# Optimization experiments

Measured on AMD Instinct MI355X. Metric: run time of the kernel, lower is better.

The kernel has to match this reference:

```python
import jax, jax.numpy as jnp
import numpy as np

EPS = 1e-5
NEG_INF = -1e30

def layer_norm(x, g, b):
    mu = jnp.mean(x, axis=-1, keepdims=True)
    var = jnp.var(x, axis=-1, keepdims=True)
    return (x - mu) * jax.lax.rsqrt(var + EPS) * g + b

def setup_inputs() -> dict:
    B, L, D, H, F = 2, 2048, 1024, 16, 4096
    key = jax.random.key(0)
    ks = jax.random.split(key, 12)
    s = 0.02
    return {
        "x": jax.random.normal(ks[0], (B, L, D), jnp.float32),
        "torus_dist": jax.random.uniform(ks[1], (1, L, L), jnp.float32),
        "time_emb": jax.random.normal(ks[2], (B, D), jnp.float32),
        "mask": jnp.ones((B, L), dtype=bool),
        "ln1_g": jnp.ones((D,), jnp.float32),
        "ln1_b": jnp.zeros((D,), jnp.float32),
        "Wqkv": jax.random.normal(ks[3], (D, 3 * D), jnp.float32) * s,
        "Wout": jax.random.normal(ks[4], (D, D), jnp.float32) * s,
        "torus_scale": jnp.full((H,), 0.1, jnp.float32),
        "ln2_g": jnp.ones((D,), jnp.float32),
        "ln2_b": jnp.zeros((D,), jnp.float32),
        "W1": jax.random.normal(ks[5], (D, F), jnp.float32) * s,
        "b1": jnp.zeros((F,), jnp.float32),
        "W2": jax.random.normal(ks[6], (F, D), jnp.float32) * s,
        "b2": jnp.zeros((D,), jnp.float32),
        "Wt": jax.random.normal(ks[7], (D, 2 * D), jnp.float32) * s,
        "bt": jnp.zeros((2 * D,), jnp.float32),
    }

def reference(x, torus_dist, time_emb, mask, ln1_g, ln1_b, Wqkv, Wout,
              torus_scale, ln2_g, ln2_b, W1, b1, W2, b2, Wt, bt):
    B, L, D = x.shape
    H = torus_scale.shape[0]
    hd = D // H
    # AdaLN time modulation
    tp = jax.nn.gelu(time_emb) @ Wt + bt          # [B, 2D]
    scale, shift = jnp.split(tp, 2, axis=-1)
    h = layer_norm(x, ln1_g, ln1_b) * (1.0 + scale[:, None, :]) + shift[:, None, :]
    # QKV: [B, L, 3, H, hd]
    qkv = (h @ Wqkv).reshape(B, L, 3, H, hd)
    q = jnp.transpose(qkv[:, :, 0], (0, 2, 1, 3))  # [B, H, L, hd]
    k = jnp.transpose(qkv[:, :, 1], (0, 2, 1, 3))
    v = jnp.transpose(qkv[:, :, 2], (0, 2, 1, 3))
    scores = jnp.einsum('bhqd,bhkd->bhqk', q, k) / np.sqrt(hd).astype(np.float32)
    scores = scores - torus_dist[:, None, :, :] * torus_scale[None, :, None, None]
    pad = ~mask[:, None, None, :]                  # [B,1,1,L]
    scores = jnp.where(pad, NEG_INF, scores)
    attn = jax.nn.softmax(scores, axis=-1)
    attn = jnp.nan_to_num(attn, nan=0.0)
    out = jnp.einsum('bhqk,bhkd->bhqd', attn, v)
    out = jnp.transpose(out, (0, 2, 1, 3)).reshape(B, L, D)
    x = x + out @ Wout
    h2 = layer_norm(x, ln2_g, ln2_b)
    x = x + (jax.nn.gelu(h2 @ W1 + b1) @ W2 + b2)
    return x
```

## Files before the change

kernel.cpp:

```cpp
#include <hip/hip_runtime.h>

typedef unsigned short us16;
typedef __bf16 bf16x8 __attribute__((ext_vector_type(8)));
typedef float f32x2 __attribute__((ext_vector_type(2)));
typedef float f32x4 __attribute__((ext_vector_type(4)));
typedef float f32x16 __attribute__((ext_vector_type(16)));
typedef unsigned u32x4 __attribute__((ext_vector_type(4)));

#define DEV __device__ __forceinline__

DEV us16 f2bf(float x) {
  union { float f; unsigned u; } un; un.f = x;
  unsigned r = un.u + 0x7fffu + ((un.u >> 16) & 1u);
  return (us16)(r >> 16);
}
DEV float bf2f(us16 u) {
  union { unsigned u; float f; } x; x.u = ((unsigned)u) << 16; return x.f;
}
DEV float gelu_f(float x) {
  float u = 0.7978845608028654f * (x + 0.044715f * x * x * x);
  float e = __expf(2.0f * u);
  return x * (1.0f - 1.0f / (e + 1.0f));
}

DEV f32x16 mfma32(bf16x8 a, bf16x8 b, f32x16 c) {
  return __builtin_amdgcn_mfma_f32_32x32x16_bf16(a, b, c, 0, 0, 0);
}

DEV unsigned cvtpk_bf16(float lo, float hi) {
  unsigned r;
  asm("v_cvt_pk_bf16_f32 %0, %1, %2" : "=v"(r) : "v"(lo), "v"(hi));
  return r;
}
DEV void plswap(unsigned& x, unsigned& y) {
  asm("v_permlane32_swap_b32 %0, %1" : "+v"(x), "+v"(y));
}

DEV void gll16(const void* gp, void* lp) {
  __builtin_amdgcn_global_load_lds(
      (__attribute__((address_space(1))) unsigned int*)(unsigned long long)(gp),
      (__attribute__((address_space(3))) unsigned int*)(unsigned int)(unsigned long long)(lp),
      16, 0, 0);
}

__global__ __launch_bounds__(256) void prep_tp(const float* __restrict__ te,
                                               const float* __restrict__ Wt,
                                               const float* __restrict__ bt,
                                               float* __restrict__ tp) {
  __shared__ float ge[1024];
  __shared__ float red[256];
  const int b = blockIdx.y, jt = blockIdx.x, t = threadIdx.x;
  for (int i = t; i < 1024; i += 256) ge[i] = gelu_f(te[b * 1024 + i]);
  __syncthreads();
  const int j = jt * 64 + (t & 63);
  const int dg = t >> 6;
  float acc = 0.f;
  for (int i = 0; i < 256; ++i) {
    int d = dg * 256 + i;
    acc += ge[d] * Wt[(size_t)d * 2048 + j];
  }
  red[t] = acc;
  __syncthreads();
  if (t < 64) tp[b * 2048 + jt * 64 + t] =
      red[t] + red[64 + t] + red[128 + t] + red[192 + t] + bt[jt * 64 + t];
}

__global__ __launch_bounds__(256) void transpose_cast(const float* __restrict__ W,
                                                      us16* __restrict__ Wo,
                                                      int K, int N) {
  __shared__ float t[32][33];
  const int bn = blockIdx.x * 32, bk = blockIdx.y * 32;
  const int tx = threadIdx.x & 31, ty = threadIdx.x >> 5;
#pragma unroll
  for (int j = 0; j < 32; j += 8) t[ty + j][tx] = W[(size_t)(bk + ty + j) * N + bn + tx];
  __syncthreads();
#pragma unroll
  for (int j = 0; j < 32; j += 8) Wo[(size_t)(bn + ty + j) * K + bk + tx] = f2bf(t[tx][ty + j]);
}

template <int MOD>
__global__ __launch_bounds__(256) void ln_kernel(const float* __restrict__ x,
                                                 const float* __restrict__ gw,
                                                 const float* __restrict__ bw,
                                                 const float* __restrict__ tp,
                                                 us16* __restrict__ out) {
  const int row = blockIdx.x, b = row >> 11, t = threadIdx.x;
  const int lane = t & 63, wid = t >> 6;
  float4 xv = ((const float4*)(x + (size_t)row * 1024))[t];
  float s = xv.x + xv.y + xv.z + xv.w;
  float s2 = xv.x * xv.x + xv.y * xv.y + xv.z * xv.z + xv.w * xv.w;
#pragma unroll
  for (int o = 32; o; o >>= 1) { s += __shfl_xor(s, o); s2 += __shfl_xor(s2, o); }
  __shared__ float rs_[4], rq_[4];
  if (lane == 0) { rs_[wid] = s; rq_[wid] = s2; }
  __syncthreads();
  s = rs_[0] + rs_[1] + rs_[2] + rs_[3];
  s2 = rq_[0] + rq_[1] + rq_[2] + rq_[3];
  const float mu = s * 0.0009765625f;
  const float var = s2 * 0.0009765625f - mu * mu;
  const float rsig = rsqrtf(var + 1e-5f);
  float4 gv = ((const float4*)gw)[t], bv = ((const float4*)bw)[t];
  float y[4] = {(xv.x - mu) * rsig * gv.x + bv.x, (xv.y - mu) * rsig * gv.y + bv.y,
                (xv.z - mu) * rsig * gv.z + bv.z, (xv.w - mu) * rsig * gv.w + bv.w};
  if (MOD) {
    float4 sc = ((const float4*)(tp + b * 2048))[t];
    float4 sh = ((const float4*)(tp + b * 2048 + 1024))[t];
    y[0] = y[0] * (1.f + sc.x) + sh.x;
    y[1] = y[1] * (1.f + sc.y) + sh.y;
    y[2] = y[2] * (1.f + sc.z) + sh.z;
    y[3] = y[3] * (1.f + sc.w) + sh.w;
  }
  ushort4 o = {f2bf(y[0]), f2bf(y[1]), f2bf(y[2]), f2bf(y[3])};
  ((ushort4*)(out + (size_t)row * 1024))[t] = o;
}

__global__ __launch_bounds__(256) void permute_dist(const float* __restrict__ dist,
                                                    us16* __restrict__ dp) {
  const int Q = blockIdx.x >> 3, part = blockIdx.x & 7;
  for (int j = threadIdx.x; j < 2048; j += 256) {
    int i = part * 2048 + j;
    int l = i & 63, ks = (i >> 6) & 7, t = i >> 9;
    int row = Q * 32 + (l & 31);
    int col = t * 64 + ks * 8 + (l >> 5) * 4;
    float4 v = *(const float4*)(dist + (size_t)row * 2048 + col);
    ushort4 o = {f2bf(v.x), f2bf(v.y), f2bf(v.z), f2bf(v.w)};
    *(ushort4*)(dp + ((size_t)Q * 16384 + i) * 4) = o;
  }
}

__global__ __launch_bounds__(256) void transpose_v(const us16* __restrict__ v,
                                                   us16* __restrict__ vt) {
  __shared__ us16 t[64][72];
  const int bh = blockIdx.y, kv0 = blockIdx.x * 64;
  const int tid = threadIdx.x;
  const int r = tid >> 2, c0 = (tid & 3) * 16;
  const us16* src = v + ((size_t)bh * 2048 + kv0 + r) * 64 + c0;
  *(uint4*)&t[r][c0] = *(const uint4*)src;
  *(uint4*)&t[r][c0 + 8] = *(const uint4*)(src + 8);
  __syncthreads();
  const int d = tid >> 2, kvl = (tid & 3) * 16;
  us16 buf[16];
#pragma unroll
  for (int i = 0; i < 16; ++i) buf[i] = t[kvl + i][d];
  us16* dst = vt + ((size_t)bh * 64 + d) * 2048 + kv0 + kvl;
  *(uint4*)dst = *(uint4*)buf;
  *(uint4*)(dst + 8) = *(uint4*)(buf + 8);
}

template <int EPI>
__global__ __launch_bounds__(256) void gemm_bt(const us16* __restrict__ A,
                                               const us16* __restrict__ Bt,
                                               int M, int N, int K,
                                               const float* __restrict__ addf,
                                               const float* __restrict__ bias,
                                               float* __restrict__ outf,
                                               us16* __restrict__ outh,
                                               us16* __restrict__ qb,
                                               us16* __restrict__ kb,
                                               us16* __restrict__ vb) {
  __shared__ us16 Al[128 * 64];
  __shared__ us16 Bl[128 * 64];
  const int tid = threadIdx.x, lane = tid & 63, wid = tid >> 6;
  const int wm = wid >> 1, wn = wid & 1;
  const int nbx = gridDim.x, nwg = nbx * gridDim.y;
  const int idlin = blockIdx.y * nbx + blockIdx.x;
  const int wg = (idlin & 7) * (nwg >> 3) + (idlin >> 3);
  const int bm = wg / nbx, bn = wg % nbx;
  const int q31 = lane & 31, hi = lane >> 5;
  const int srow = lane >> 3;
  const int scol = ((lane & 7) ^ srow) << 3;

  f32x16 acc[2][2] = {};
  const size_t arow0 = (size_t)bm * 128 + wid * 32 + srow;
  const size_t brow0 = (size_t)bn * 128 + wid * 32 + srow;

  for (int k0 = 0; k0 < K; k0 += 64) {
#pragma unroll
    for (int j = 0; j < 4; ++j) {
      gll16(A + (arow0 + j * 8) * K + k0 + scol, (char*)Al + (wid * 32 + j * 8) * 128);
      gll16(Bt + (brow0 + j * 8) * K + k0 + scol, (char*)Bl + (wid * 32 + j * 8) * 128);
    }
    __syncthreads();
#pragma unroll
    for (int ks = 0; ks < 4; ++ks) {
      const int cb = ks * 32 + hi * 16;
      bf16x8 af[2], bfr[2];
#pragma unroll
      for (int i = 0; i < 2; ++i) {
        int ra = wm * 64 + i * 32 + q31;
        af[i] = *(const bf16x8*)((const char*)Al + ra * 128 + (cb ^ ((ra & 7) << 4)));
        int rb = wn * 64 + i * 32 + q31;
        bfr[i] = *(const bf16x8*)((const char*)Bl + rb * 128 + (cb ^ ((rb & 7) << 4)));
      }
#pragma unroll
      for (int mi = 0; mi < 2; ++mi)
#pragma unroll
        for (int ni = 0; ni < 2; ++ni)
          acc[mi][ni] = mfma32(af[mi], bfr[ni], acc[mi][ni]);
    }
    __syncthreads();
  }

#pragma unroll
  for (int mi = 0; mi < 2; ++mi)
#pragma unroll
    for (int ni = 0; ni < 2; ++ni)
#pragma unroll
      for (int r = 0; r < 16; ++r) {
        int grow = bm * 128 + wm * 64 + mi * 32 + (r & 3) + 8 * (r >> 2) + 4 * hi;
        int gcol = bn * 128 + wn * 64 + ni * 32 + q31;
        float v = acc[mi][ni][r];
        if (EPI == 0) {
          int b = grow >> 11, lseq = grow & 2047;
          int which = gcol >> 10, hc = gcol & 1023;
          int hh = hc >> 6, d = hc & 63;
          size_t o = ((size_t)(b * 16 + hh) * 2048 + lseq) * 64 + d;
          if (which == 0) qb[o] = f2bf(v * 0.1803368801f);
          else if (which == 1) kb[o] = f2bf(v);
          else vb[o] = f2bf(v);
        } else if (EPI == 1) {
          outh[(size_t)grow * N + gcol] = f2bf(gelu_f(v + bias[gcol]));
        } else if (EPI == 2) {
          size_t o = (size_t)grow * N + gcol;
          outf[o] = addf[o] + v;
        } else {
          size_t o = (size_t)grow * N + gcol;
          outf[o] = addf[o] + bias[gcol] + v;
        }
      }
}

typedef union { f32x16 v; f32x2 p[8]; float f[16]; } F16U;

__global__ __launch_bounds__(256) void attn_kernel(const us16* __restrict__ q,
                                                   const us16* __restrict__ k,
                                                   const us16* __restrict__ vt,
                                                   const us16* __restrict__ dp,
                                                   const float* __restrict__ tscale,
                                                   us16* __restrict__ ctx) {
  __shared__ __align__(16) us16 Kl[2][64 * 64];
  __shared__ __align__(16) us16 Vl[2][64 * 64];
  __shared__ float als[128];
  const int tid = threadIdx.x, l = tid & 63, w4 = tid >> 6;
  const int q31 = l & 31, hi = l >> 5;
  const int qt = blockIdx.x, bh = blockIdx.y;
  const int b = bh >> 4, hh = bh & 15;
  const float scaleL = tscale[hh] * 1.44269504f;
  const int srow = l >> 3;
  const int scol = ((l & 7) ^ srow) << 3;
  const int q0blk = qt * 128;

  const us16* qg = q + ((size_t)bh * 2048 + q0blk + w4 * 32 + q31) * 64;
  bf16x8 qf[4];
#pragma unroll
  for (int kd = 0; kd < 4; ++kd) qf[kd] = *(const bf16x8*)(qg + kd * 16 + hi * 8);

  const us16* kpb = k + (size_t)bh * 2048 * 64;
  const us16* vpb = vt + (size_t)bh * 64 * 2048;
  const us16* dpw = dp + ((size_t)(qt * 4 + w4) * 16384 + l) * 4;

  f32x16 Oa = {}, Ob = {};
  float m = -1e30f, lsum = 0.f;
  ushort4 dA[8], dB[8];

  auto stage = [&](int kvn, int bufsel) {
#pragma unroll
    for (int j = 0; j < 2; ++j) {
      int row = w4 * 16 + j * 8 + srow;
      gll16(kpb + (size_t)(kvn + row) * 64 + scol, (char*)&Kl[bufsel][0] + (w4 * 16 + j * 8) * 128);
      gll16(vpb + (size_t)row * 2048 + kvn + scol, (char*)&Vl[bufsel][0] + (w4 * 16 + j * 8) * 128);
    }
  };
  auto load_d = [&](ushort4* dst, int t) {
#pragma unroll
    for (int ks = 0; ks < 8; ++ks) dst[ks] = *(const ushort4*)(dpw + (t * 8 + ks) * 256);
  };

  auto tile = [&](const us16* Kb, const us16* Vb, const ushort4* dc) {
    f32x16 SAv = {}, SBv = {};
#pragma unroll
    for (int kd = 0; kd < 4; ++kd) {
      const int cb = kd * 32 + hi * 16;
      const int r0 = q31, r1 = 32 + q31;
      bf16x8 ka = *(const bf16x8*)((const char*)Kb + r0 * 128 + (cb ^ ((r0 & 7) << 4)));
      bf16x8 kb2 = *(const bf16x8*)((const char*)Kb + r1 * 128 + (cb ^ ((r1 & 7) << 4)));
      SAv = mfma32(ka, qf[kd], SAv);
      SBv = mfma32(kb2, qf[kd], SBv);
    }
    F16U A, B2;
    A.v = SAv;
    B2.v = SBv;

    f32x2 t0 = __builtin_elementwise_max(__builtin_elementwise_max(A.p[0], A.p[1]),
                                         __builtin_elementwise_max(A.p[2], A.p[3]));
    f32x2 t1 = __builtin_elementwise_max(__builtin_elementwise_max(A.p[4], A.p[5]),
                                         __builtin_elementwise_max(A.p[6], A.p[7]));
    f32x2 t2 = __builtin_elementwise_max(__builtin_elementwise_max(B2.p[0], B2.p[1]),
                                         __builtin_elementwise_max(B2.p[2], B2.p[3]));
    f32x2 t3 = __builtin_elementwise_max(__builtin_elementwise_max(B2.p[4], B2.p[5]),
                                         __builtin_elementwise_max(B2.p[6], B2.p[7]));
    f32x2 tt = __builtin_elementwise_max(__builtin_elementwise_max(t0, t1),
                                         __builtin_elementwise_max(t2, t3));
    float pm = fmaxf(tt[0], tt[1]);
    pm = fmaxf(pm, __shfl_xor(pm, 32));

    if (__any(pm > m + 11.53f)) {
      float mn = fmaxf(m, pm);
      float al = __builtin_exp2f(m - mn);
      m = mn;
      lsum *= al;
      if (!hi) als[w4 * 32 + q31] = al;
      f32x4 av[4];
#pragma unroll
      for (int g2 = 0; g2 < 4; ++g2) av[g2] = *(const f32x4*)&als[w4 * 32 + g2 * 8 + hi * 4];
#pragma unroll
      for (int g2 = 0; g2 < 4; ++g2)
#pragma unroll
        for (int e = 0; e < 4; ++e) {
          Oa[g2 * 4 + e] *= av[g2][e];
          Ob[g2 * 4 + e] *= av[g2][e];
        }
    }

    f32x2 nm = {-m, -m};
    f32x2 ns = {-scaleL, -scaleL};
#pragma unroll
    for (int ks = 0; ks < 4; ++ks) {
      ushort4 dlo = dc[ks], dhi = dc[ks + 4];
      f32x2 l0 = {bf2f(dlo.x), bf2f(dlo.y)};
      f32x2 l1 = {bf2f(dlo.z), bf2f(dlo.w)};
      f32x2 h0 = {bf2f(dhi.x), bf2f(dhi.y)};
      f32x2 h1 = {bf2f(dhi.z), bf2f(dhi.w)};
      A.p[ks * 2] = __builtin_elementwise_fma(ns, l0, A.p[ks * 2] + nm);
      A.p[ks * 2 + 1] = __builtin_elementwise_fma(ns, l1, A.p[ks * 2 + 1] + nm);
      B2.p[ks * 2] = __builtin_elementwise_fma(ns, h0, B2.p[ks * 2] + nm);
      B2.p[ks * 2 + 1] = __builtin_elementwise_fma(ns, h1, B2.p[ks * 2 + 1] + nm);
    }
#pragma unroll
    for (int i = 0; i < 16; ++i) {
      A.f[i] = __builtin_exp2f(A.f[i]);
      B2.f[i] = __builtin_exp2f(B2.f[i]);
    }

    f32x2 s = ((A.p[0] + A.p[1]) + (A.p[2] + A.p[3])) + ((A.p[4] + A.p[5]) + (A.p[6] + A.p[7]));
    s = s + (((B2.p[0] + B2.p[1]) + (B2.p[2] + B2.p[3])) +
             ((B2.p[4] + B2.p[5]) + (B2.p[6] + B2.p[7])));
    float rs = s[0] + s[1];
    rs += __shfl_xor(rs, 32);
    lsum += rs;

#pragma unroll
    for (int ks = 0; ks < 4; ++ks) {
      float p0, p1, p2, p3, p4, p5, p6, p7;
      if (ks == 0) { p0=A.f[0];p1=A.f[1];p2=A.f[2];p3=A.f[3];p4=A.f[4];p5=A.f[5];p6=A.f[6];p7=A.f[7]; }
      else if (ks == 1) { p0=A.f[8];p1=A.f[9];p2=A.f[10];p3=A.f[11];p4=A.f[12];p5=A.f[13];p6=A.f[14];p7=A.f[15]; }
      else if (ks == 2) { p0=B2.f[0];p1=B2.f[1];p2=B2.f[2];p3=B2.f[3];p4=B2.f[4];p5=B2.f[5];p6=B2.f[6];p7=B2.f[7]; }
      else { p0=B2.f[8];p1=B2.f[9];p2=B2.f[10];p3=B2.f[11];p4=B2.f[12];p5=B2.f[13];p6=B2.f[14];p7=B2.f[15]; }
      unsigned a = cvtpk_bf16(p0, p1), c = cvtpk_bf16(p2, p3);
      unsigned bb = cvtpk_bf16(p4, p5), dd = cvtpk_bf16(p6, p7);
      plswap(a, bb);
      plswap(c, dd);
      u32x4 fw;
      fw[0] = a; fw[1] = c; fw[2] = bb; fw[3] = dd;
      bf16x8 pf = __builtin_bit_cast(bf16x8, fw);
      const int cb = ks * 32 + hi * 16;
      const int rv0 = q31, rv1 = 32 + q31;
      bf16x8 v0 = *(const bf16x8*)((const char*)Vb + rv0 * 128 + (cb ^ ((rv0 & 7) << 4)));
      Oa = mfma32(pf, v0, Oa);
      bf16x8 v1 = *(const bf16x8*)((const char*)Vb + rv1 * 128 + (cb ^ ((rv1 & 7) << 4)));
      Ob = mfma32(pf, v1, Ob);
    }
  };

  stage(0, 0);
  load_d(dA, 0);
  __syncthreads();

  for (int t = 0; t < 32; t += 2) {
    stage((t + 1) * 64, 1);
    load_d(dB, t + 1);
    tile(&Kl[0][0], &Vl[0][0], dA);
    __syncthreads();
    if (t + 2 < 32) {
      stage((t + 2) * 64, 0);
      load_d(dA, t + 2);
    }
    tile(&Kl[1][0], &Vl[1][0], dB);
    __syncthreads();
  }

  float rl = 1.f / lsum;
  if (!hi) als[w4 * 32 + q31] = rl;
  f32x4 rv[4];
#pragma unroll
  for (int g2 = 0; g2 < 4; ++g2) rv[g2] = *(const f32x4*)&als[w4 * 32 + g2 * 8 + hi * 4];
  us16* cb_ = ctx + ((size_t)b * 2048 + q0blk + w4 * 32) * 1024 + hh * 64;
#pragma unroll
  for (int g2 = 0; g2 < 4; ++g2)
#pragma unroll
    for (int e = 0; e < 4; ++e) {
      int r = g2 * 4 + e;
      int qrow = g2 * 8 + hi * 4 + e;
      cb_[(size_t)qrow * 1024 + q31] = f2bf(Oa[r] * rv[g2][e]);
      cb_[(size_t)qrow * 1024 + 32 + q31] = f2bf(Ob[r] * rv[g2][e]);
    }
}

extern "C" void kernel_launch(void* const* d_in, const int* in_sizes, int n_in,
                              void* d_out, int out_size, void* d_ws, size_t ws_size,
                              hipStream_t stream) {
  const float* x    = (const float*)d_in[0];
  const float* dist = (const float*)d_in[1];
  const float* te   = (const float*)d_in[2];
  const float* ln1g = (const float*)d_in[4];
  const float* ln1b = (const float*)d_in[5];
  const float* Wqkv = (const float*)d_in[6];
  const float* Wout = (const float*)d_in[7];
  const float* tsc  = (const float*)d_in[8];
  const float* ln2g = (const float*)d_in[9];
  const float* ln2b = (const float*)d_in[10];
  const float* W1   = (const float*)d_in[11];
  const float* b1   = (const float*)d_in[12];
  const float* W2   = (const float*)d_in[13];
  const float* b2   = (const float*)d_in[14];
  const float* Wtm  = (const float*)d_in[15];
  const float* btm  = (const float*)d_in[16];
  float* out = (float*)d_out;
  (void)in_sizes; (void)n_in; (void)out_size; (void)ws_size;

  char* w = (char*)d_ws;
  size_t off = 0;
  auto alloc = [&](size_t bytes) { size_t o = off; off += (bytes + 255) & ~(size_t)255; return o; };
  float* tp  = (float*)(w + alloc((size_t)2 * 2048 * 4));
  us16* h    = (us16*)(w + alloc((size_t)4096 * 1024 * 2));
  us16* wqkvT= (us16*)(w + alloc((size_t)3072 * 1024 * 2));
  us16* woutT= (us16*)(w + alloc((size_t)1024 * 1024 * 2));
  us16* w1T  = (us16*)(w + alloc((size_t)4096 * 1024 * 2));
  us16* w2T  = (us16*)(w + alloc((size_t)1024 * 4096 * 2));
  us16* qb   = (us16*)(w + alloc((size_t)4 * 4096 * 1024 * 2));
  us16* kb   = qb + (size_t)4096 * 1024;
  us16* vb   = kb + (size_t)4096 * 1024;
  us16* vtb  = vb + (size_t)4096 * 1024;
  us16* gbuf = qb;
  us16* dp   = (us16*)(w + alloc((size_t)2048 * 2048 * 2));
  us16* ctx  = (us16*)(w + alloc((size_t)4096 * 1024 * 2));
  float* x1  = (float*)(w + alloc((size_t)4096 * 1024 * 4));
  us16* h2   = (us16*)(w + alloc((size_t)4096 * 1024 * 2));

  prep_tp<<<dim3(32, 2), 256, 0, stream>>>(te, Wtm, btm, tp);
  transpose_cast<<<dim3(96, 32), 256, 0, stream>>>(Wqkv, wqkvT, 1024, 3072);
  transpose_cast<<<dim3(32, 32), 256, 0, stream>>>(Wout, woutT, 1024, 1024);
  transpose_cast<<<dim3(128, 32), 256, 0, stream>>>(W1, w1T, 1024, 4096);
  transpose_cast<<<dim3(32, 128), 256, 0, stream>>>(W2, w2T, 4096, 1024);
  ln_kernel<1><<<4096, 256, 0, stream>>>(x, ln1g, ln1b, tp, h);
  permute_dist<<<512, 256, 0, stream>>>(dist, dp);
  gemm_bt<0><<<dim3(24, 32), 256, 0, stream>>>(h, wqkvT, 4096, 3072, 1024,
                                               nullptr, nullptr, nullptr, nullptr, qb, kb, vb);
  transpose_v<<<dim3(32, 32), 256, 0, stream>>>(vb, vtb);
  attn_kernel<<<dim3(16, 32), 256, 0, stream>>>(qb, kb, vtb, dp, tsc, ctx);
  gemm_bt<2><<<dim3(8, 32), 256, 0, stream>>>(ctx, woutT, 4096, 1024, 1024,
                                              x, nullptr, x1, nullptr, nullptr, nullptr, nullptr);
  ln_kernel<0><<<4096, 256, 0, stream>>>(x1, ln2g, ln2b, nullptr, h2);
  gemm_bt<1><<<dim3(32, 32), 256, 0, stream>>>(h2, w1T, 4096, 4096, 1024,
                                               nullptr, b1, nullptr, gbuf, nullptr, nullptr, nullptr);
  gemm_bt<3><<<dim3(8, 32), 256, 0, stream>>>(gbuf, w2T, 4096, 1024, 4096,
                                              x1, b2, out, nullptr, nullptr, nullptr, nullptr);
}
```

Baseline: 311.3 us.

## Split attention KV range and MLP2 K dimension across two workgroups

```diff
diff --git a/kernel.cpp b/kernel.cpp
--- a/kernel.cpp
+++ b/kernel.cpp
@@ -174,7 +174,10 @@
   const size_t arow0 = (size_t)bm * 128 + wid * 32 + srow;
   const size_t brow0 = (size_t)bn * 128 + wid * 32 + srow;
 
-  for (int k0 = 0; k0 < K; k0 += 64) {
+  int kbeg = 0, kend = K;
+  if (EPI == 4) { kbeg = blockIdx.z * (K >> 1); kend = kbeg + (K >> 1); }
+
+  for (int k0 = kbeg; k0 < kend; k0 += 64) {
 #pragma unroll
     for (int j = 0; j < 4; ++j) {
       gll16(A + (arow0 + j * 8) * K + k0 + scol, (char*)Al + (wid * 32 + j * 8) * 128);
@@ -200,6 +203,9 @@
     }
     __syncthreads();
   }
+
+  us16* pd = nullptr;
+  if (EPI == 4) pd = blockIdx.z == 0 ? outh : qb;
 
 #pragma unroll
   for (int mi = 0; mi < 2; ++mi)
@@ -223,6 +229,8 @@
         } else if (EPI == 2) {
           size_t o = (size_t)grow * N + gcol;
           outf[o] = addf[o] + v;
+        } else if (EPI == 4) {
+          pd[(size_t)grow * N + gcol] = f2bf(v);
         } else {
           size_t o = (size_t)grow * N + gcol;
           outf[o] = addf[o] + bias[gcol] + v;
@@ -230,6 +238,25 @@
       }
 }
 
+__global__ __launch_bounds__(256) void combine_mlp2(const float* __restrict__ x1,
+                                                    const float* __restrict__ b2,
+                                                    const us16* __restrict__ p0,
+                                                    const us16* __restrict__ p1,
+                                                    float* __restrict__ out) {
+  const int row = blockIdx.x, t = threadIdx.x;
+  const size_t base = (size_t)row * 1024 + t * 4;
+  float4 xv = *(const float4*)(x1 + base);
+  float4 bv = *(const float4*)(b2 + t * 4);
+  ushort4 a = *(const ushort4*)(p0 + base);
+  ushort4 b = *(const ushort4*)(p1 + base);
+  float4 o;
+  o.x = xv.x + bv.x + bf2f(a.x) + bf2f(b.x);
+  o.y = xv.y + bv.y + bf2f(a.y) + bf2f(b.y);
+  o.z = xv.z + bv.z + bf2f(a.z) + bf2f(b.z);
+  o.w = xv.w + bv.w + bf2f(a.w) + bf2f(b.w);
+  *(float4*)(out + base) = o;
+}
+
 typedef union { f32x16 v; f32x2 p[8]; float f[16]; } F16U;
 
 __global__ __launch_bounds__(256) void attn_kernel(const us16* __restrict__ q,
@@ -237,18 +264,20 @@
                                                    const us16* __restrict__ vt,
                                                    const us16* __restrict__ dp,
                                                    const float* __restrict__ tscale,
-                                                   us16* __restrict__ ctx) {
+                                                   us16* __restrict__ opart,
+                                                   float2* __restrict__ mlp) {
   __shared__ __align__(16) us16 Kl[2][64 * 64];
   __shared__ __align__(16) us16 Vl[2][64 * 64];
   __shared__ float als[128];
   const int tid = threadIdx.x, l = tid & 63, w4 = tid >> 6;
   const int q31 = l & 31, hi = l >> 5;
-  const int qt = blockIdx.x, bh = blockIdx.y;
+  const int qt = blockIdx.x >> 1, g = blockIdx.x & 1, bh = blockIdx.y;
   const int b = bh >> 4, hh = bh & 15;
   const float scaleL = tscale[hh] * 1.44269504f;
   const int srow = l >> 3;
   const int scol = ((l & 7) ^ srow) << 3;
   const int q0blk = qt * 128;
+  const int kvbase = g * 1024;
 
   const us16* qg = q + ((size_t)bh * 2048 + q0blk + w4 * 32 + q31) * 64;
   bf16x8 qf[4];
@@ -271,9 +300,9 @@
       gll16(vpb + (size_t)row * 2048 + kvn + scol, (char*)&Vl[bufsel][0] + (w4 * 16 + j * 8) * 128);
     }
   };
-  auto load_d = [&](ushort4* dst, int t) {
-#pragma unroll
-    for (int ks = 0; ks < 8; ++ks) dst[ks] = *(const ushort4*)(dpw + (t * 8 + ks) * 256);
+  auto load_d = [&](ushort4* dst, int tabs) {
+#pragma unroll
+    for (int ks = 0; ks < 8; ++ks) dst[ks] = *(const ushort4*)(dpw + (tabs * 8 + ks) * 256);
   };
 
   auto tile = [&](const us16* Kb, const us16* Vb, const ushort4* dc) {
@@ -372,38 +401,66 @@
     }
   };
 
-  stage(0, 0);
-  load_d(dA, 0);
+  stage(kvbase, 0);
+  load_d(dA, g * 16);
   __syncthreads();
 
-  for (int t = 0; t < 32; t += 2) {
-    stage((t + 1) * 64, 1);
-    load_d(dB, t + 1);
+  for (int t = 0; t < 16; t += 2) {
+    stage(kvbase + (t + 1) * 64, 1);
+    load_d(dB, g * 16 + t + 1);
     tile(&Kl[0][0], &Vl[0][0], dA);
     __syncthreads();
-    if (t + 2 < 32) {
-      stage((t + 2) * 64, 0);
-      load_d(dA, t + 2);
+    if (t + 2 < 16) {
+      stage(kvbase + (t + 2) * 64, 0);
+      load_d(dA, g * 16 + t + 2);
     }
     tile(&Kl[1][0], &Vl[1][0], dB);
     __syncthreads();
   }
 
   float rl = 1.f / lsum;
-  if (!hi) als[w4 * 32 + q31] = rl;
+  if (!hi) {
+    als[w4 * 32 + q31] = rl;
+    mlp[((size_t)g * 32 + bh) * 2048 + q0blk + w4 * 32 + q31] = make_float2(m, lsum);
+  }
   f32x4 rv[4];
 #pragma unroll
   for (int g2 = 0; g2 < 4; ++g2) rv[g2] = *(const f32x4*)&als[w4 * 32 + g2 * 8 + hi * 4];
-  us16* cb_ = ctx + ((size_t)b * 2048 + q0blk + w4 * 32) * 1024 + hh * 64;
+  us16* ob_ = opart + ((size_t)g * 4096 + b * 2048 + q0blk + w4 * 32) * 1024 + hh * 64;
 #pragma unroll
   for (int g2 = 0; g2 < 4; ++g2)
 #pragma unroll
     for (int e = 0; e < 4; ++e) {
       int r = g2 * 4 + e;
       int qrow = g2 * 8 + hi * 4 + e;
-      cb_[(size_t)qrow * 1024 + q31] = f2bf(Oa[r] * rv[g2][e]);
-      cb_[(size_t)qrow * 1024 + 32 + q31] = f2bf(Ob[r] * rv[g2][e]);
-    }
+      ob_[(size_t)qrow * 1024 + q31] = f2bf(Oa[r] * rv[g2][e]);
+      ob_[(size_t)qrow * 1024 + 32 + q31] = f2bf(Ob[r] * rv[g2][e]);
+    }
+}
+
+__global__ __launch_bounds__(256) void attn_merge(const us16* __restrict__ opart,
+                                                  const float2* __restrict__ mlp,
+                                                  us16* __restrict__ ctx) {
+  const int row = blockIdx.x;
+  const int t = threadIdx.x;
+  const int d0 = t * 4, hh = d0 >> 6;
+  const int b = row >> 11, lq = row & 2047;
+  const int bh = b * 16 + hh;
+  float2 v0 = mlp[(size_t)bh * 2048 + lq];
+  float2 v1 = mlp[((size_t)32 + bh) * 2048 + lq];
+  float mt = fmaxf(v0.x, v1.x);
+  float a0 = __builtin_exp2f(v0.x - mt) * v0.y;
+  float a1 = __builtin_exp2f(v1.x - mt) * v1.y;
+  float inv = 1.f / (a0 + a1);
+  float w0 = a0 * inv, w1 = a1 * inv;
+  ushort4 o0 = *(const ushort4*)&opart[(size_t)row * 1024 + d0];
+  ushort4 o1 = *(const ushort4*)&opart[((size_t)4096 + row) * 1024 + d0];
+  ushort4 o;
+  o.x = f2bf(w0 * bf2f(o0.x) + w1 * bf2f(o1.x));
+  o.y = f2bf(w0 * bf2f(o0.y) + w1 * bf2f(o1.y));
+  o.z = f2bf(w0 * bf2f(o0.z) + w1 * bf2f(o1.z));
+  o.w = f2bf(w0 * bf2f(o0.w) + w1 * bf2f(o1.w));
+  *(ushort4*)&ctx[(size_t)row * 1024 + d0] = o;
 }
 
 extern "C" void kernel_launch(void* const* d_in, const int* in_sizes, int n_in,
@@ -446,6 +503,10 @@
   us16* ctx  = (us16*)(w + alloc((size_t)4096 * 1024 * 2));
   float* x1  = (float*)(w + alloc((size_t)4096 * 1024 * 4));
   us16* h2   = (us16*)(w + alloc((size_t)4096 * 1024 * 2));
+  float2* mlb = (float2*)(w + alloc((size_t)2 * 32 * 2048 * 8));
+  us16* opart = (us16*)x1;
+  us16* mp0 = dp;
+  us16* mp1 = ctx;
 
   prep_tp<<<dim3(32, 2), 256, 0, stream>>>(te, Wtm, btm, tp);
   transpose_cast<<<dim3(96, 32), 256, 0, stream>>>(Wqkv, wqkvT, 1024, 3072);
@@ -457,12 +518,14 @@
   gemm_bt<0><<<dim3(24, 32), 256, 0, stream>>>(h, wqkvT, 4096, 3072, 1024,
                                                nullptr, nullptr, nullptr, nullptr, qb, kb, vb);
   transpose_v<<<dim3(32, 32), 256, 0, stream>>>(vb, vtb);
-  attn_kernel<<<dim3(16, 32), 256, 0, stream>>>(qb, kb, vtb, dp, tsc, ctx);
+  attn_kernel<<<dim3(32, 32), 256, 0, stream>>>(qb, kb, vtb, dp, tsc, opart, mlb);
+  attn_merge<<<4096, 256, 0, stream>>>(opart, mlb, ctx);
   gemm_bt<2><<<dim3(8, 32), 256, 0, stream>>>(ctx, woutT, 4096, 1024, 1024,
                                               x, nullptr, x1, nullptr, nullptr, nullptr, nullptr);
   ln_kernel<0><<<4096, 256, 0, stream>>>(x1, ln2g, ln2b, nullptr, h2);
   gemm_bt<1><<<dim3(32, 32), 256, 0, stream>>>(h2, w1T, 4096, 4096, 1024,
                                                nullptr, b1, nullptr, gbuf, nullptr, nullptr, nullptr);
-  gemm_bt<3><<<dim3(8, 32), 256, 0, stream>>>(gbuf, w2T, 4096, 1024, 4096,
-                                              x1, b2, out, nullptr, nullptr, nullptr, nullptr);
-}
+  gemm_bt<4><<<dim3(8, 32, 2), 256, 0, stream>>>(gbuf, w2T, 4096, 1024, 4096,
+                                                 nullptr, nullptr, nullptr, mp0, mp1, nullptr, nullptr);
+  combine_mlp2<<<4096, 256, 0, stream>>>(x1, b2, mp0, mp1, out);
+}
```

Result: faster. 302.5 us (-2.8%).

## Split-K the second MLP GEMM and triple-buffer attention K/V staging

Applied to the files above, without the earlier changes.

```diff
diff --git a/kernel.cpp b/kernel.cpp
--- a/kernel.cpp
+++ b/kernel.cpp
@@ -174,7 +174,10 @@
   const size_t arow0 = (size_t)bm * 128 + wid * 32 + srow;
   const size_t brow0 = (size_t)bn * 128 + wid * 32 + srow;
 
-  for (int k0 = 0; k0 < K; k0 += 64) {
+  int kbeg = 0, kend = K;
+  if (EPI == 4) { kbeg = blockIdx.z * (K >> 1); kend = kbeg + (K >> 1); }
+
+  for (int k0 = kbeg; k0 < kend; k0 += 64) {
 #pragma unroll
     for (int j = 0; j < 4; ++j) {
       gll16(A + (arow0 + j * 8) * K + k0 + scol, (char*)Al + (wid * 32 + j * 8) * 128);
@@ -200,6 +203,9 @@
     }
     __syncthreads();
   }
+
+  us16* pd = nullptr;
+  if (EPI == 4) pd = blockIdx.z == 0 ? outh : qb;
 
 #pragma unroll
   for (int mi = 0; mi < 2; ++mi)
@@ -223,11 +229,32 @@
         } else if (EPI == 2) {
           size_t o = (size_t)grow * N + gcol;
           outf[o] = addf[o] + v;
+        } else if (EPI == 4) {
+          pd[(size_t)grow * N + gcol] = f2bf(v);
         } else {
           size_t o = (size_t)grow * N + gcol;
           outf[o] = addf[o] + bias[gcol] + v;
         }
       }
+}
+
+__global__ __launch_bounds__(256) void combine_mlp2(const float* __restrict__ x1,
+                                                    const float* __restrict__ b2,
+                                                    const us16* __restrict__ p0,
+                                                    const us16* __restrict__ p1,
+                                                    float* __restrict__ out) {
+  const int row = blockIdx.x, t = threadIdx.x;
+  const size_t base = (size_t)row * 1024 + t * 4;
+  float4 xv = *(const float4*)(x1 + base);
+  float4 bv = *(const float4*)(b2 + t * 4);
+  ushort4 a = *(const ushort4*)(p0 + base);
+  ushort4 b = *(const ushort4*)(p1 + base);
+  float4 o;
+  o.x = xv.x + bv.x + bf2f(a.x) + bf2f(b.x);
+  o.y = xv.y + bv.y + bf2f(a.y) + bf2f(b.y);
+  o.z = xv.z + bv.z + bf2f(a.z) + bf2f(b.z);
+  o.w = xv.w + bv.w + bf2f(a.w) + bf2f(b.w);
+  *(float4*)(out + base) = o;
 }
 
 typedef union { f32x16 v; f32x2 p[8]; float f[16]; } F16U;
@@ -238,8 +265,8 @@
                                                    const us16* __restrict__ dp,
                                                    const float* __restrict__ tscale,
                                                    us16* __restrict__ ctx) {
-  __shared__ __align__(16) us16 Kl[2][64 * 64];
-  __shared__ __align__(16) us16 Vl[2][64 * 64];
+  __shared__ __align__(16) us16 Kl[3][64 * 64];
+  __shared__ __align__(16) us16 Vl[3][64 * 64];
   __shared__ float als[128];
   const int tid = threadIdx.x, l = tid & 63, w4 = tid >> 6;
   const int q31 = l & 31, hi = l >> 5;
@@ -271,9 +298,9 @@
       gll16(vpb + (size_t)row * 2048 + kvn + scol, (char*)&Vl[bufsel][0] + (w4 * 16 + j * 8) * 128);
     }
   };
-  auto load_d = [&](ushort4* dst, int t) {
-#pragma unroll
-    for (int ks = 0; ks < 8; ++ks) dst[ks] = *(const ushort4*)(dpw + (t * 8 + ks) * 256);
+  auto load_d = [&](ushort4* dst, int tabs) {
+#pragma unroll
+    for (int ks = 0; ks < 8; ++ks) dst[ks] = *(const ushort4*)(dpw + (tabs * 8 + ks) * 256);
   };
 
   auto tile = [&](const us16* Kb, const us16* Vb, const ushort4* dc) {
@@ -374,19 +401,28 @@
 
   stage(0, 0);
   load_d(dA, 0);
-  __syncthreads();
+  stage(64, 1);
+  load_d(dB, 1);
 
   for (int t = 0; t < 32; t += 2) {
-    stage((t + 1) * 64, 1);
-    load_d(dB, t + 1);
-    tile(&Kl[0][0], &Vl[0][0], dA);
-    __syncthreads();
+    asm volatile("s_waitcnt vmcnt(12)" ::: "memory");
+    __builtin_amdgcn_s_barrier();
     if (t + 2 < 32) {
-      stage((t + 2) * 64, 0);
+      stage((t + 2) * 64, (t + 2) % 3);
       load_d(dA, t + 2);
     }
-    tile(&Kl[1][0], &Vl[1][0], dB);
-    __syncthreads();
+    tile(&Kl[t % 3][0], &Vl[t % 3][0], dA);
+    if (t + 1 == 31) {
+      asm volatile("s_waitcnt vmcnt(0)" ::: "memory");
+    } else {
+      asm volatile("s_waitcnt vmcnt(12)" ::: "memory");
+    }
+    __builtin_amdgcn_s_barrier();
+    if (t + 3 < 32) {
+      stage((t + 3) * 64, (t + 3) % 3);
+      load_d(dB, t + 3);
+    }
+    tile(&Kl[(t + 1) % 3][0], &Vl[(t + 1) % 3][0], dB);
   }
 
   float rl = 1.f / lsum;
@@ -446,6 +482,8 @@
   us16* ctx  = (us16*)(w + alloc((size_t)4096 * 1024 * 2));
   float* x1  = (float*)(w + alloc((size_t)4096 * 1024 * 4));
   us16* h2   = (us16*)(w + alloc((size_t)4096 * 1024 * 2));
+  us16* mp0  = dp;
+  us16* mp1  = ctx;
 
   prep_tp<<<dim3(32, 2), 256, 0, stream>>>(te, Wtm, btm, tp);
   transpose_cast<<<dim3(96, 32), 256, 0, stream>>>(Wqkv, wqkvT, 1024, 3072);
@@ -463,6 +501,7 @@
   ln_kernel<0><<<4096, 256, 0, stream>>>(x1, ln2g, ln2b, nullptr, h2);
   gemm_bt<1><<<dim3(32, 32), 256, 0, stream>>>(h2, w1T, 4096, 4096, 1024,
                                                nullptr, b1, nullptr, gbuf, nullptr, nullptr, nullptr);
-  gemm_bt<3><<<dim3(8, 32), 256, 0, stream>>>(gbuf, w2T, 4096, 1024, 4096,
-                                              x1, b2, out, nullptr, nullptr, nullptr, nullptr);
-}
+  gemm_bt<4><<<dim3(8, 32, 2), 256, 0, stream>>>(gbuf, w2T, 4096, 1024, 4096,
+                                                 nullptr, nullptr, nullptr, mp0, mp1, nullptr, nullptr);
+  combine_mlp2<<<4096, 256, 0, stream>>>(x1, b2, mp0, mp1, out);
+}
```

After: 305.9 us. Within noise of the previous version (-1.7%).
